# Kernel optimization log

Hardware: AMD Instinct MI355X
Metric: run time of the kernel (lower is better)

## Reference

```python
import jax, jax.numpy as jnp
import numpy as np
import math

B, Hs, Ws, C, NH, PP = 4, 32, 32, 1024, 16, 128
N = Hs * Ws
HD = C // NH
MAX_REL = 32
ROPE_THETA = 10000.0


def _gelu(t):
    return jax.nn.gelu(t, approximate=False)  # torch nn.GELU default (erf)


def _rope(x):
    # x: [B, nh, N, hd]; interleaved even/odd rotation as in _apply_rope
    hd = x.shape[-1]
    inv_freq = 1.0 / (ROPE_THETA ** (jnp.arange(0, hd, 2, dtype=jnp.float32) / hd))
    pos = jnp.arange(x.shape[-2], dtype=jnp.float32)
    ang = pos[:, None] * inv_freq[None, :]  # [N, hd/2]
    sin, cos = jnp.sin(ang), jnp.cos(ang)
    x1, x2 = x[..., 0::2], x[..., 1::2]
    return jnp.stack([x1 * cos - x2 * sin, x2 * cos + x1 * sin], axis=-1).reshape(x.shape)


def _rel_bias(table):
    # static index computation (numpy), gather from learned table -> [1, NH, N, N]
    coords = np.arange(Hs)
    cy, cx = np.meshgrid(coords, coords, indexing='ij')
    cf = np.stack([cy.reshape(-1), cx.reshape(-1)])  # [2, N]
    rel = cf[:, :, None] - cf[:, None, :]            # [2, N, N]
    idx = (rel[0] + MAX_REL - 1) * (2 * MAX_REL - 1) + (rel[1] + MAX_REL - 1)
    return table[jnp.asarray(idx.reshape(-1))].reshape(N, N, NH).transpose(2, 0, 1)[None]


def setup_inputs() -> dict:
    key = jax.random.key(0)
    ks = iter(jax.random.split(key, 40))
    def w(shape, s=0.02):
        return jax.random.normal(next(ks), shape, jnp.float32) * s
    return dict(
        x=jax.random.normal(next(ks), (B, N, C), jnp.float32),
        plucker=jax.random.normal(next(ks), (B, Hs, Ws, 6), jnp.float32),
        w_qkv=w((C, 3 * C)), w_self_proj=w((C, C)), b_self_proj=jnp.zeros((C,), jnp.float32),
        pl_w1=w((6, 2 * PP)), pl_b1=jnp.zeros((2 * PP,), jnp.float32),
        pl_w2=w((2 * PP, PP)), pl_b2=jnp.zeros((PP,), jnp.float32),
        pl_w3=w((PP, PP)), pl_b3=jnp.zeros((PP,), jnp.float32),
        w_cq=w((C, C)), w_pk=w((PP, C)), w_pv=w((PP, C)),
        w_cross_proj=w((C, C)), b_cross_proj=jnp.zeros((C,), jnp.float32),
        ray_dir_bias=w((NH,)),
        ds_w1=w((6, 4 * NH)), ds_b1=jnp.zeros((4 * NH,), jnp.float32),
        ds_w2=w((4 * NH, NH)), ds_b2=jnp.zeros((NH,), jnp.float32),
        gb_w1=w((2 * PP, C // 2)), gb_b1=jnp.zeros((C // 2,), jnp.float32),
        gb_w2=w((C // 2, NH)), gb_b2=jnp.zeros((NH,), jnp.float32),
        rel_table=w(((2 * MAX_REL - 1) ** 2, NH)),
        gfe_w1=w((C + PP, C)), gfe_b1=jnp.zeros((C,), jnp.float32),
        gfe_w2=w((C, C)), gfe_b2=jnp.zeros((C,), jnp.float32),
    )


def reference(x, plucker, w_qkv, w_self_proj, b_self_proj,
              pl_w1, pl_b1, pl_w2, pl_b2, pl_w3, pl_b3,
              w_cq, w_pk, w_pv, w_cross_proj, b_cross_proj,
              ray_dir_bias, ds_w1, ds_b1, ds_w2, ds_b2,
              gb_w1, gb_b1, gb_w2, gb_b2, rel_table,
              gfe_w1, gfe_b1, gfe_w2, gfe_b2):
    scale = HD ** (-0.5)
    pl_flat = plucker.reshape(B, N, 6)

    # ---- self attention with RoPE + relative position bias ----
    qkv = (x @ w_qkv).reshape(B, N, 3, NH, HD).transpose(2, 0, 3, 1, 4)
    q, k, v = qkv[0], qkv[1], qkv[2]          # [B, NH, N, HD]
    q, k = _rope(q), _rope(k)
    attn = jnp.einsum('bhnd,bhmd->bhnm', q, k) * scale + _rel_bias(rel_table)
    attn = jax.nn.softmax(attn, axis=-1)
    sa = jnp.einsum('bhnm,bhmd->bhnd', attn, v).transpose(0, 2, 1, 3).reshape(B, N, C)
    sa = sa @ w_self_proj + b_self_proj

    # ---- plucker mlp embedding ----
    pp = _gelu(pl_flat @ pl_w1 + pl_b1)
    pp = _gelu(pp @ pl_w2 + pl_b2)
    pp = pp @ pl_w3 + pl_b3                   # [B, N, PP]

    # ---- cross attention (features -> plucker) with geometric biases ----
    cq = (sa @ w_cq).reshape(B, N, NH, HD).transpose(0, 2, 1, 3)
    ck = (pp @ w_pk).reshape(B, N, NH, HD).transpose(0, 2, 1, 3)
    cv = (pp @ w_pv).reshape(B, N, NH, HD).transpose(0, 2, 1, 3)
    cq, ck = _rope(cq), _rope(ck)
    ca = jnp.einsum('bhnd,bhmd->bhnm', cq, ck) * scale

    # ray direction similarity bias (per-head learned weight)
    d = pl_flat[..., :3]
    dn = d / jnp.maximum(jnp.linalg.norm(d, axis=-1, keepdims=True), 1e-12)
    sim = jnp.einsum('bnd,bmd->bnm', dn, dn)  # [B, N, N]
    ca = ca + sim[:, None, :, :] * ray_dir_bias[None, :, None, None]

    # distance-aware per-query multiplicative scale
    ds = jnp.tanh(_gelu(pl_flat @ ds_w1 + ds_b1) @ ds_w2 + ds_b2)  # [B, N, NH]
    ca = ca * (1.0 + ds.transpose(0, 2, 1)[..., None])

    # geometric attention bias from spatial diffs of plucker features
    p2 = pp.reshape(B, Hs, Ws, PP)
    hdiff = jnp.pad(jnp.abs(p2[:, :, 1:] - p2[:, :, :-1]), ((0, 0), (0, 0), (0, 1), (0, 0)))
    vdiff = jnp.pad(jnp.abs(p2[:, 1:] - p2[:, :-1]), ((0, 0), (0, 1), (0, 0), (0, 0)))
    sd = jnp.concatenate([hdiff, vdiff], axis=-1).reshape(B, N, 2 * PP)
    gb = jnp.tanh(_gelu(sd @ gb_w1 + gb_b1) @ gb_w2 + gb_b2)  # [B, N, NH]
    ca = ca + gb.transpose(0, 2, 1)[:, :, None, :]            # broadcast over queries

    ca = jax.nn.softmax(ca, axis=-1)
    co = jnp.einsum('bhnm,bhmd->bhnd', ca, cv).transpose(0, 2, 1, 3).reshape(B, N, C)
    co = co @ w_cross_proj + b_cross_proj

    # ---- geometric feature enhancement + residual ----
    enh = _gelu(jnp.concatenate([co, pp], axis=-1) @ gfe_w1 + gfe_b1) @ gfe_w2 + gfe_b2
    return enh + x
```

## Files before the change

### kernel.cpp

```cpp
#include <hip/hip_runtime.h>
#include <math.h>

#define B_ 4
#define N_ 1024
#define C_ 1024
#define NH_ 16
#define HD_ 64
#define PP_ 128
#define LOG2E 1.4426950408889634f

typedef __bf16 bf16;
typedef __attribute__((ext_vector_type(8))) __bf16 bf16x8;
typedef __attribute__((ext_vector_type(4))) __bf16 bf16x4;
typedef __attribute__((ext_vector_type(4))) float f32x4;

#define MFMA_BF16(a, b, c) __builtin_amdgcn_mfma_f32_16x16x32_bf16((a), (b), (c), 0, 0, 0)

__device__ __forceinline__ float gelu_f(float x) {
    return 0.5f * x * (1.0f + erff(x * 0.70710678118654752f));
}

__device__ __forceinline__ void gload16(const void* g, void* l) {
    __builtin_amdgcn_global_load_lds(
        (const __attribute__((address_space(1))) void*)g,
        (__attribute__((address_space(3))) void*)l, 16, 0, 0);
}

__device__ __forceinline__ void stage64(const bf16* __restrict__ g, int pitchB,
                                        bf16* lds, int t) {
    int row = t >> 3, c = t & 7;
    const char* src = (const char*)g + (size_t)row * pitchB + ((c ^ (row & 7)) << 4);
    gload16(src, lds + (size_t)(t & 448) * 8);
}

__device__ __forceinline__ void stage32(const bf16* __restrict__ g, bf16* lds, int t) {
    if (t < 256) {
        int row = t >> 3, c = t & 7;
        const char* src = (const char*)g + (size_t)row * 128 + ((c ^ (row & 7)) << 4);
        gload16(src, lds + (size_t)(t & 192) * 8);
    }
}

__device__ __forceinline__ bf16x8 lds8_swz(const bf16* lds, int row, int colb) {
    return *reinterpret_cast<const bf16x8*>(
        (const char*)lds + row * 128 + (colb ^ ((row & 7) << 4)));
}

__device__ __forceinline__ bf16x8 lds8_ke(const bf16* lds, int kr, int g) {
    int r = kr >> 1;
    int ch = ((kr & 1) * 4 + g) ^ (r & 7);
    return *reinterpret_cast<const bf16x8*>((const char*)lds + r * 128 + (ch << 4));
}

__global__ __launch_bounds__(256) void rope_tab_k(float2* __restrict__ rt)
{
    int g = blockIdx.x * 256 + threadIdx.x;
    const int n = g >> 5, i = g & 31;
    const float inv = powf(10000.0f, -(float)(2 * i) / 64.0f);
    const float ang = (float)n * inv;
    rt[g] = make_float2(cosf(ang), sinf(ang));
}

__global__ __launch_bounds__(256) void relT_k(const float* __restrict__ rel_table,
                                              float* __restrict__ relT)
{
    int g = blockIdx.x * 256 + threadIdx.x;
    if (g >= 16 * 3969) return;
    int h = g / 3969, idx = g - h * 3969;
    relT[g] = rel_table[idx * 16 + h];
}

struct TJobs {
    const float* src[11];
    bf16* dst[11];
    int K[11];
    int N[11];
};

__global__ __launch_bounds__(256) void tcast_k(TJobs J)
{
    const int j = blockIdx.z;
    const int Kd = J.K[j], Nd = J.N[j];
    const int n0 = blockIdx.x * 32, k0 = blockIdx.y * 32;
    if (n0 >= Nd || k0 >= Kd) return;
    __shared__ float tl[32][33];
    const int t = threadIdx.x, tx = t & 31, ty = t >> 5;
    const float* src = J.src[j];
    bf16* dst = J.dst[j];
    #pragma unroll
    for (int r = 0; r < 4; ++r) {
        int kk = ty + r * 8;
        tl[kk][tx] = src[(size_t)(k0 + kk) * Nd + n0 + tx];
    }
    __syncthreads();
    #pragma unroll
    for (int r = 0; r < 4; ++r) {
        int nn = ty + r * 8;
        dst[(size_t)(n0 + nn) * Kd + k0 + tx] = (bf16)tl[tx][nn];
    }
}

__global__ __launch_bounds__(256) void cast_rm(const float* __restrict__ in,
                                               bf16* __restrict__ out, int n4)
{
    int g = blockIdx.x * 256 + threadIdx.x;
    if (g >= n4) return;
    float4 v = reinterpret_cast<const float4*>(in)[g];
    bf16x4 o = {(bf16)v.x, (bf16)v.y, (bf16)v.z, (bf16)v.w};
    reinterpret_cast<bf16x4*>(out)[g] = o;
}

template<int NI, int BK>
__global__ __launch_bounds__(256) void gemm_m(
    const bf16* __restrict__ A, const bf16* __restrict__ A2,
    const bf16* __restrict__ Bt, const bf16* __restrict__ Bt2,
    const float* __restrict__ bias, const float* __restrict__ resid,
    void* __restrict__ out0, void* __restrict__ out1, void* __restrict__ out2,
    const float2* __restrict__ rtab,
    int M, int N, int K, int K1A, int K1B, int epi, int act_gelu, float scale)
{
    __shared__ bf16 As[2][128 * BK];
    __shared__ bf16 Bs[2][NI * 32 * BK];
    const int t = threadIdx.x;
    const int w = t >> 6, lane = t & 63;
    const int row0 = blockIdx.y * 128, col0 = blockIdx.x * (NI * 32);
    const int wm = w >> 1, wn = w & 1;
    const int K2A = K - K1A, K2B = K - K1B;
    f32x4 acc[4][NI];
    #pragma unroll
    for (int mi = 0; mi < 4; ++mi)
        #pragma unroll
        for (int ni = 0; ni < NI; ++ni)
            acc[mi][ni] = (f32x4){0.f, 0.f, 0.f, 0.f};

    #define STAGE_AB32(k0, buf)                                                \
        {                                                                      \
            _Pragma("unroll")                                                  \
            for (int r = 0; r < 2; ++r) {                                      \
                int c = r * 256 + t;                                           \
                int rr = c >> 2, koff = (c & 3) * 8;                           \
                const bf16* srca = ((k0) < K1A)                                \
                    ? A + (size_t)(row0 + rr) * K1A + (k0) + koff              \
                    : A2 + (size_t)(row0 + rr) * K2A + ((k0) - K1A) + koff;    \
                gload16(srca, As[buf] + (size_t)(r * 256 + (t & 192)) * 8);    \
            }                                                                  \
            _Pragma("unroll")                                                  \
            for (int r = 0; r < NI / 2; ++r) {                                 \
                int c = r * 256 + t;                                           \
                int rr = c >> 2, koff = (c & 3) * 8;                           \
                const bf16* srcb = ((k0) < K1B)                                \
                    ? Bt + (size_t)(col0 + rr) * K1B + (k0) + koff             \
                    : Bt2 + (size_t)(col0 + rr) * K2B + ((k0) - K1B) + koff;   \
                gload16(srcb, Bs[buf] + (size_t)(r * 256 + (t & 192)) * 8);    \
            }                                                                  \
        }

    #define STAGE_AB64(k0, buf)                                                \
        {                                                                      \
            const bf16* abase; int apitch;                                     \
            if ((k0) < K1A) { abase = A + (k0); apitch = K1A; }                \
            else            { abase = A2 + ((k0) - K1A); apitch = K2A; }       \
            _Pragma("unroll")                                                  \
            for (int r = 0; r < 4; ++r) {                                      \
                int c = r * 256 + t;                                           \
                int rr = c >> 3, cc = c & 7;                                   \
                const char* srca = (const char*)(abase + (size_t)(row0 + rr) * apitch) \
                                   + ((cc ^ (rr & 7)) << 4);                   \
                gload16(srca, As[buf] + (size_t)(r * 256 + (t & 192)) * 8);    \
            }                                                                  \
            const bf16* bbase; int bpitch;                                     \
            if ((k0) < K1B) { bbase = Bt + (k0); bpitch = K1B; }               \
            else            { bbase = Bt2 + ((k0) - K1B); bpitch = K2B; }      \
            _Pragma("unroll")                                                  \
            for (int r = 0; r < NI; ++r) {                                     \
                int c = r * 256 + t;                                           \
                int rr = c >> 3, cc = c & 7;                                   \
                const char* srcb = (const char*)(bbase + (size_t)(col0 + rr) * bpitch) \
                                   + ((cc ^ (rr & 7)) << 4);                   \
                gload16(srcb, Bs[buf] + (size_t)(r * 256 + (t & 192)) * 8);    \
            }                                                                  \
        }

    int cur = 0;
    const int nk = K / BK;
    if constexpr (BK == 32) {
        STAGE_AB32(0, 0);
        __syncthreads();
        for (int kk = 0; kk < nk; ++kk) {
            if (kk + 1 < nk) STAGE_AB32((kk + 1) * 32, cur ^ 1);
            bf16x8 af[4], bfv[NI];
            #pragma unroll
            for (int mi = 0; mi < 4; ++mi)
                af[mi] = *reinterpret_cast<const bf16x8*>(
                    As[cur] + (wm * 64 + mi * 16 + (lane & 15)) * 32 + (lane >> 4) * 8);
            #pragma unroll
            for (int ni = 0; ni < NI; ++ni)
                bfv[ni] = *reinterpret_cast<const bf16x8*>(
                    Bs[cur] + (wn * (NI * 16) + ni * 16 + (lane & 15)) * 32 + (lane >> 4) * 8);
            #pragma unroll
            for (int mi = 0; mi < 4; ++mi)
                #pragma unroll
                for (int ni = 0; ni < NI; ++ni)
                    acc[mi][ni] = MFMA_BF16(af[mi], bfv[ni], acc[mi][ni]);
            __syncthreads();
            cur ^= 1;
        }
    } else {
        STAGE_AB64(0, 0);
        __syncthreads();
        for (int kk = 0; kk < nk; ++kk) {
            if (kk + 1 < nk) STAGE_AB64((kk + 1) * 64, cur ^ 1);
            bf16x8 af[4][2], bfv[NI][2];
            #pragma unroll
            for (int mi = 0; mi < 4; ++mi)
                #pragma unroll
                for (int kh = 0; kh < 2; ++kh)
                    af[mi][kh] = lds8_swz(As[cur], wm * 64 + mi * 16 + (lane & 15),
                                          kh * 64 + (lane >> 4) * 16);
            #pragma unroll
            for (int ni = 0; ni < NI; ++ni)
                #pragma unroll
                for (int kh = 0; kh < 2; ++kh)
                    bfv[ni][kh] = lds8_swz(Bs[cur], wn * (NI * 16) + ni * 16 + (lane & 15),
                                           kh * 64 + (lane >> 4) * 16);
            #pragma unroll
            for (int kh = 0; kh < 2; ++kh)
                #pragma unroll
                for (int mi = 0; mi < 4; ++mi)
                    #pragma unroll
                    for (int ni = 0; ni < NI; ++ni)
                        acc[mi][ni] = MFMA_BF16(af[mi][kh], bfv[ni][kh], acc[mi][ni]);
            __syncthreads();
            cur ^= 1;
        }
    }
    #undef STAGE_AB32
    #undef STAGE_AB64

    #pragma unroll
    for (int mi = 0; mi < 4; ++mi) {
        #pragma unroll
        for (int ni = 0; ni < NI; ++ni) {
            const int col = col0 + wn * (NI * 16) + ni * 16 + (lane & 15);
            if (epi <= 1 || epi == 5) {
                const float bv = bias ? bias[col] : 0.f;
                #pragma unroll
                for (int j = 0; j < 4; ++j) {
                    const int row = row0 + wm * 64 + mi * 16 + (lane >> 4) * 4 + j;
                    float v = acc[mi][ni][j] + bv;
                    if (act_gelu) v = gelu_f(v);
                    if (epi == 0) {
                        if (resid) v += resid[(size_t)row * N + col];
                        ((float*)out0)[(size_t)row * N + col] = v;
                    } else if (epi == 1) {
                        ((bf16*)out0)[(size_t)row * N + col] = (bf16)v;
                    } else {
                        ((float*)out0)[(size_t)row * N + col] = v;
                        ((bf16*)out1)[(size_t)row * N + col] = (bf16)v;
                    }
                }
            } else if (epi == 2) {
                const int reg = col >> 10;
                const int h = (col >> 6) & 15, d = col & 63;
                if (reg <= 1) {
                    bf16* dst = reg == 0 ? (bf16*)out0 : (bf16*)out1;
                    const float sc = reg == 0 ? scale : 1.0f;
                    #pragma unroll
                    for (int j = 0; j < 4; ++j) {
                        const int row = row0 + wm * 64 + mi * 16 + (lane >> 4) * 4 + j;
                        const int b = row >> 10, n = row & 1023;
                        float v = acc[mi][ni][j];
                        float pv = __shfl_xor(v, 1);
                        float2 cs = rtab[(n << 5) + (d >> 1)];
                        float o = (d & 1) == 0 ? v * cs.x - pv * cs.y
                                               : v * cs.x + pv * cs.y;
                        dst[((size_t)((b * 16 + h) * 1024 + n)) * 64 + d] = (bf16)(o * sc);
                    }
                } else {
                    bf16x4 o4;
                    #pragma unroll
                    for (int j = 0; j < 4; ++j) o4[j] = (bf16)acc[mi][ni][j];
                    const int row = row0 + wm * 64 + mi * 16 + (lane >> 4) * 4;
                    const int b = row >> 10, n = row & 1023;
                    *reinterpret_cast<bf16x4*>(
                        (bf16*)out2 + ((size_t)((b * 16 + h) * 64 + d)) * 1024 + n) = o4;
                }
            } else if (epi == 3 || epi == 6) {
                const int h = (col >> 6) & 15, d = col & 63;
                #pragma unroll
                for (int j = 0; j < 4; ++j) {
                    const int row = row0 + wm * 64 + mi * 16 + (lane >> 4) * 4 + j;
                    const int b = row >> 10, n = row & 1023;
                    float v = acc[mi][ni][j];
                    float pv = __shfl_xor(v, 1);
                    float2 cs = rtab[(n << 5) + (d >> 1)];
                    float o = (d & 1) == 0 ? v * cs.x - pv * cs.y
                                           : v * cs.x + pv * cs.y;
                    float sc = scale;
                    if (epi == 6) sc *= 1.0f + resid[(size_t)row * 16 + h];
                    ((bf16*)out0)[((size_t)((b * 16 + h) * 1024 + n)) * 64 + d] = (bf16)(o * sc);
                }
            } else {
                const int h = (col >> 6) & 15, d = col & 63;
                bf16x4 o4;
                #pragma unroll
                for (int j = 0; j < 4; ++j) o4[j] = (bf16)acc[mi][ni][j];
                const int row = row0 + wm * 64 + mi * 16 + (lane >> 4) * 4;
                const int b = row >> 10, n = row & 1023;
                *reinterpret_cast<bf16x4*>(
                    (bf16*)out0 + ((size_t)((b * 16 + h) * 64 + d)) * 1024 + n) = o4;
            }
        }
    }
}

__global__ __launch_bounds__(256) void extfill_k(
    const float* __restrict__ dn, const float* __restrict__ ds,
    const float* __restrict__ gb, const float* __restrict__ rdb,
    bf16* __restrict__ qe, bf16* __restrict__ ke)
{
    int g = blockIdx.x * 256 + threadIdx.x;
    if (g >= 65536) return;
    const int bh = g >> 10, n = g & 1023;
    const int b = bh >> 4, h = bh & 15;
    const size_t rn = (size_t)b * 1024 + n;
    const float c1 = rdb[h] * LOG2E * (1.0f + ds[rn * 16 + h]);
    const float dx = dn[rn * 4], dy = dn[rn * 4 + 1], dz = dn[rn * 4 + 2];
    bf16x8 z = {};
    bf16x8 q0 = z, k0 = z;
    q0[0] = (bf16)(dx * c1); q0[1] = (bf16)(dy * c1); q0[2] = (bf16)(dz * c1); q0[3] = (bf16)1.0f;
    k0[0] = (bf16)dx; k0[1] = (bf16)dy; k0[2] = (bf16)dz; k0[3] = (bf16)(gb[rn * 16 + h] * LOG2E);
    bf16x8* qp = reinterpret_cast<bf16x8*>(qe + (size_t)g * 32);
    bf16x8* kp = reinterpret_cast<bf16x8*>(ke + (size_t)g * 32);
    qp[0] = q0; qp[1] = z; qp[2] = z; qp[3] = z;
    kp[0] = k0; kp[1] = z; kp[2] = z; kp[3] = z;
}

__device__ __forceinline__ void attn_bid(int bid, int& bh, int& r0t) {
    const int xcd = bid & 7, s = bid >> 3;
    bh = (s >> 3) * 8 + xcd;
    r0t = s & 7;
}

__global__ __launch_bounds__(512) void attn_self_m(
    const bf16* __restrict__ qb, const bf16* __restrict__ kb, const bf16* __restrict__ vtb,
    const float* __restrict__ relT, bf16* __restrict__ sab)
{
    __shared__ bf16 Ks[2][64 * 64];
    __shared__ bf16 Vs[2][80 * 64];
    __shared__ bf16 Ps[128 * 64];
    __shared__ float relb[2][320];
    const int t = threadIdx.x, w = t >> 6, lane = t & 63;
    int bh, r0t;
    attn_bid(blockIdx.x, bh, r0t);
    const int b = bh >> 4, h = bh & 15, r0 = r0t * 128;
    const float* relTh = relT + h * 3969;
    const int y0 = r0 >> 5;

    {
        const bf16* g = qb + ((size_t)bh * 1024 + r0) * 64;
        #pragma unroll
        for (int r = 0; r < 2; ++r) {
            int i = r * 512 + t;
            int row = i >> 3, c = i & 7;
            const char* src = (const char*)g + (size_t)row * 128 + ((c ^ (row & 7)) << 4);
            gload16(src, Ps + (size_t)(r * 512 + (t & 448)) * 8);
        }
    }
    __syncthreads();
    bf16x8 aq[2];
    {
        const int qr = w * 16 + (lane & 15);
        aq[0] = lds8_swz(Ps, qr, (lane >> 4) * 16);
        aq[1] = lds8_swz(Ps, qr, 64 + (lane >> 4) * 16);
    }
    for (int i = t; i < 2048; i += 512) {
        int buf = i >> 10, idx = i & 1023;
        int row = 64 + (idx >> 6), col = idx & 63;
        Vs[buf][row * 64 + col] = (row == 64) ? (bf16)1.0f : (bf16)0.0f;
    }
    __syncthreads();
    stage64(kb + (size_t)bh * 65536, 128, Ks[0], t);
    stage64(vtb + (size_t)bh * 65536, 2048, Vs[0], t);
    if (t < 320) relb[0][t] = LOG2E * relTh[(y0 + 30 + (t >> 6)) * 63 + min(t & 63, 62)];

    float m_run[4];
    f32x4 of[4], ofe;
    #pragma unroll
    for (int j = 0; j < 4; ++j) m_run[j] = -3e38f;
    #pragma unroll
    for (int dt = 0; dt < 4; ++dt) of[dt] = (f32x4){0.f, 0.f, 0.f, 0.f};
    ofe = (f32x4){0.f, 0.f, 0.f, 0.f};

    const int qrow_lo = (lane >> 4) * 4;
    int dybase[4];
    #pragma unroll
    for (int j = 0; j < 4; ++j) {
        int qg = r0 + w * 16 + qrow_lo + j;
        dybase[j] = (((qg >> 5) - y0) + 1) * 64 + (qg & 31) + 31;
    }
    __syncthreads();

    int cur = 0;
    for (int mt = 0; mt < 16; ++mt) {
        if (mt < 15) {
            stage64(kb + (size_t)bh * 65536 + (size_t)(mt + 1) * 64 * 64, 128, Ks[cur ^ 1], t);
            stage64(vtb + (size_t)bh * 65536 + (size_t)(mt + 1) * 64, 2048, Vs[cur ^ 1], t);
            if (t < 320)
                relb[cur ^ 1][t] = LOG2E * relTh[(y0 - 2 * (mt + 1) + 30 + (t >> 6)) * 63 + min(t & 63, 62)];
        }
        f32x4 sf[4];
        __builtin_amdgcn_s_setprio(1);
        #pragma unroll
        for (int ct = 0; ct < 4; ++ct) {
            const int kr = ct * 16 + (lane & 15);
            f32x4 a = (f32x4){0.f, 0.f, 0.f, 0.f};
            a = MFMA_BF16(aq[0], lds8_swz(Ks[cur], kr, (lane >> 4) * 16), a);
            a = MFMA_BF16(aq[1], lds8_swz(Ks[cur], kr, 64 + (lane >> 4) * 16), a);
            sf[ct] = a;
        }
        __builtin_amdgcn_s_setprio(0);
        float p[4][4], lmax[4];
        #pragma unroll
        for (int j = 0; j < 4; ++j) lmax[j] = -3e38f;
        #pragma unroll
        for (int ct = 0; ct < 4; ++ct) {
            const int xm = (ct & 1) * 16 + (lane & 15);
            const int ro = (ct >> 1) * 64 + xm;
            #pragma unroll
            for (int j = 0; j < 4; ++j) {
                float s = sf[ct][j] + relb[cur][dybase[j] - ro];
                p[ct][j] = s;
                lmax[j] = fmaxf(lmax[j], s);
            }
        }
        bool need = false;
        #pragma unroll
        for (int j = 0; j < 4; ++j) need |= (lmax[j] > m_run[j] + 8.0f);
        if (__any(need)) {
            float mx[4], alpha[4];
            #pragma unroll
            for (int j = 0; j < 4; ++j) mx[j] = lmax[j];
            #pragma unroll
            for (int d = 1; d < 16; d <<= 1)
                #pragma unroll
                for (int j = 0; j < 4; ++j) mx[j] = fmaxf(mx[j], __shfl_xor(mx[j], d));
            #pragma unroll
            for (int j = 0; j < 4; ++j) {
                float mn = fmaxf(m_run[j], mx[j]);
                alpha[j] = exp2f(m_run[j] - mn);
                m_run[j] = mn;
            }
            #pragma unroll
            for (int dt = 0; dt < 4; ++dt)
                #pragma unroll
                for (int j = 0; j < 4; ++j) of[dt][j] *= alpha[j];
            #pragma unroll
            for (int j = 0; j < 4; ++j) ofe[j] *= alpha[j];
        }
        #pragma unroll
        for (int ct = 0; ct < 4; ++ct)
            #pragma unroll
            for (int j = 0; j < 4; ++j)
                p[ct][j] = exp2f(p[ct][j] - m_run[j]);
        #pragma unroll
        for (int ct = 0; ct < 4; ++ct)
            #pragma unroll
            for (int j = 0; j < 4; ++j) {
                const int prow = w * 16 + qrow_lo + j;
                const int ch = (ct * 2 + ((lane & 15) >> 3)) ^ (prow & 7);
                *reinterpret_cast<bf16*>((char*)Ps + prow * 128 + (ch << 4) + (lane & 7) * 2)
                    = (bf16)p[ct][j];
            }
        asm volatile("s_waitcnt lgkmcnt(0)" ::: "memory");
        __builtin_amdgcn_sched_barrier(0);
        bf16x8 ap0 = lds8_swz(Ps, w * 16 + (lane & 15), (lane >> 4) * 16);
        bf16x8 ap1 = lds8_swz(Ps, w * 16 + (lane & 15), 64 + (lane >> 4) * 16);
        __builtin_amdgcn_s_setprio(1);
        #pragma unroll
        for (int dt = 0; dt < 4; ++dt) {
            const int vr = dt * 16 + (lane & 15);
            of[dt] = MFMA_BF16(ap0, lds8_swz(Vs[cur], vr, (lane >> 4) * 16), of[dt]);
            of[dt] = MFMA_BF16(ap1, lds8_swz(Vs[cur], vr, 64 + (lane >> 4) * 16), of[dt]);
        }
        {
            const int vr = 64 + (lane & 15);
            ofe = MFMA_BF16(ap0, lds8_swz(Vs[cur], vr, (lane >> 4) * 16), ofe);
            ofe = MFMA_BF16(ap1, lds8_swz(Vs[cur], vr, 64 + (lane >> 4) * 16), ofe);
        }
        __builtin_amdgcn_s_setprio(0);
        __syncthreads();
        cur ^= 1;
    }
    float inv[4];
    #pragma unroll
    for (int j = 0; j < 4; ++j) inv[j] = 1.f / __shfl(ofe[j], lane & 48);
    #pragma unroll
    for (int dt = 0; dt < 4; ++dt)
        #pragma unroll
        for (int j = 0; j < 4; ++j)
            sab[((size_t)(b * N_ + r0 + w * 16 + qrow_lo + j)) * C_ + h * 64 + dt * 16 + (lane & 15)] =
                (bf16)(of[dt][j] * inv[j]);
}

__global__ __launch_bounds__(512) void attn_cross_m(
    const bf16* __restrict__ cq, const bf16* __restrict__ qe,
    const bf16* __restrict__ ck, const bf16* __restrict__ ke,
    const bf16* __restrict__ cvt, bf16* __restrict__ cob)
{
    __shared__ bf16 Ks[2][64 * 64];
    __shared__ bf16 Ke[2][32 * 64];
    __shared__ bf16 Vs[2][80 * 64];
    __shared__ bf16 Ps[128 * 64];
    const int t = threadIdx.x, w = t >> 6, lane = t & 63;
    int bh, r0t;
    attn_bid(blockIdx.x, bh, r0t);
    const int b = bh >> 4, h = bh & 15, r0 = r0t * 128;

    {
        const bf16* g = cq + ((size_t)bh * 1024 + r0) * 64;
        #pragma unroll
        for (int r = 0; r < 2; ++r) {
            int i = r * 512 + t;
            int row = i >> 3, c = i & 7;
            const char* src = (const char*)g + (size_t)row * 128 + ((c ^ (row & 7)) << 4);
            gload16(src, Ps + (size_t)(r * 512 + (t & 448)) * 8);
        }
    }
    stage64(qe + ((size_t)bh * 1024 + r0) * 32, 128, Ks[0], t);
    __syncthreads();
    bf16x8 aq[2], aqe;
    {
        const int qr = w * 16 + (lane & 15);
        aq[0] = lds8_swz(Ps, qr, (lane >> 4) * 16);
        aq[1] = lds8_swz(Ps, qr, 64 + (lane >> 4) * 16);
        aqe = lds8_ke(Ks[0], qr, lane >> 4);
    }
    for (int i = t; i < 2048; i += 512) {
        int buf = i >> 10, idx = i & 1023;
        int row = 64 + (idx >> 6), col = idx & 63;
        Vs[buf][row * 64 + col] = (row == 64) ? (bf16)1.0f : (bf16)0.0f;
    }
    __syncthreads();
    stage64(ck + (size_t)bh * 65536, 128, Ks[0], t);
    stage32(ke + (size_t)bh * 32768, Ke[0], t);
    stage64(cvt + (size_t)bh * 65536, 2048, Vs[0], t);

    float m_run[4];
    f32x4 of[4], ofe;
    #pragma unroll
    for (int j = 0; j < 4; ++j) m_run[j] = -3e38f;
    #pragma unroll
    for (int dt = 0; dt < 4; ++dt) of[dt] = (f32x4){0.f, 0.f, 0.f, 0.f};
    ofe = (f32x4){0.f, 0.f, 0.f, 0.f};
    const int qrow_lo = (lane >> 4) * 4;
    __syncthreads();

    int cur = 0;
    for (int mt = 0; mt < 16; ++mt) {
        if (mt < 15) {
            stage64(ck + (size_t)bh * 65536 + (size_t)(mt + 1) * 64 * 64, 128, Ks[cur ^ 1], t);
            stage32(ke + (size_t)bh * 32768 + (size_t)(mt + 1) * 64 * 32, Ke[cur ^ 1], t);
            stage64(cvt + (size_t)bh * 65536 + (size_t)(mt + 1) * 64, 2048, Vs[cur ^ 1], t);
        }
        f32x4 sf[4];
        __builtin_amdgcn_s_setprio(1);
        #pragma unroll
        for (int ct = 0; ct < 4; ++ct) {
            const int kr = ct * 16 + (lane & 15);
            f32x4 a = (f32x4){0.f, 0.f, 0.f, 0.f};
            a = MFMA_BF16(aq[0], lds8_swz(Ks[cur], kr, (lane >> 4) * 16), a);
            a = MFMA_BF16(aq[1], lds8_swz(Ks[cur], kr, 64 + (lane >> 4) * 16), a);
            a = MFMA_BF16(aqe, lds8_ke(Ke[cur], kr, lane >> 4), a);
            sf[ct] = a;
        }
        __builtin_amdgcn_s_setprio(0);
        float lmax[4];
        #pragma unroll
        for (int j = 0; j < 4; ++j)
            lmax[j] = fmaxf(fmaxf(sf[0][j], sf[1][j]), fmaxf(sf[2][j], sf[3][j]));
        bool need = false;
        #pragma unroll
        for (int j = 0; j < 4; ++j) need |= (lmax[j] > m_run[j] + 8.0f);
        if (__any(need)) {
            float mx[4], alpha[4];
            #pragma unroll
            for (int j = 0; j < 4; ++j) mx[j] = lmax[j];
            #pragma unroll
            for (int d = 1; d < 16; d <<= 1)
                #pragma unroll
                for (int j = 0; j < 4; ++j) mx[j] = fmaxf(mx[j], __shfl_xor(mx[j], d));
            #pragma unroll
            for (int j = 0; j < 4; ++j) {
                float mn = fmaxf(m_run[j], mx[j]);
                alpha[j] = exp2f(m_run[j] - mn);
                m_run[j] = mn;
            }
            #pragma unroll
            for (int dt = 0; dt < 4; ++dt)
                #pragma unroll
                for (int j = 0; j < 4; ++j) of[dt][j] *= alpha[j];
            #pragma unroll
            for (int j = 0; j < 4; ++j) ofe[j] *= alpha[j];
        }
        #pragma unroll
        for (int ct = 0; ct < 4; ++ct)
            #pragma unroll
            for (int j = 0; j < 4; ++j)
                sf[ct][j] = exp2f(sf[ct][j] - m_run[j]);
        #pragma unroll
        for (int ct = 0; ct < 4; ++ct)
            #pragma unroll
            for (int j = 0; j < 4; ++j) {
                const int prow = w * 16 + qrow_lo + j;
                const int ch = (ct * 2 + ((lane & 15) >> 3)) ^ (prow & 7);
                *reinterpret_cast<bf16*>((char*)Ps + prow * 128 + (ch << 4) + (lane & 7) * 2)
                    = (bf16)sf[ct][j];
            }
        asm volatile("s_waitcnt lgkmcnt(0)" ::: "memory");
        __builtin_amdgcn_sched_barrier(0);
        bf16x8 ap0 = lds8_swz(Ps, w * 16 + (lane & 15), (lane >> 4) * 16);
        bf16x8 ap1 = lds8_swz(Ps, w * 16 + (lane & 15), 64 + (lane >> 4) * 16);
        __builtin_amdgcn_s_setprio(1);
        #pragma unroll
        for (int dt = 0; dt < 4; ++dt) {
            const int vr = dt * 16 + (lane & 15);
            of[dt] = MFMA_BF16(ap0, lds8_swz(Vs[cur], vr, (lane >> 4) * 16), of[dt]);
            of[dt] = MFMA_BF16(ap1, lds8_swz(Vs[cur], vr, 64 + (lane >> 4) * 16), of[dt]);
        }
        {
            const int vr = 64 + (lane & 15);
            ofe = MFMA_BF16(ap0, lds8_swz(Vs[cur], vr, (lane >> 4) * 16), ofe);
            ofe = MFMA_BF16(ap1, lds8_swz(Vs[cur], vr, 64 + (lane >> 4) * 16), ofe);
        }
        __builtin_amdgcn_s_setprio(0);
        __syncthreads();
        cur ^= 1;
    }
    float inv[4];
    #pragma unroll
    for (int j = 0; j < 4; ++j) inv[j] = 1.f / __shfl(ofe[j], lane & 48);
    #pragma unroll
    for (int dt = 0; dt < 4; ++dt)
        #pragma unroll
        for (int j = 0; j < 4; ++j)
            cob[((size_t)(b * N_ + r0 + w * 16 + qrow_lo + j)) * C_ + h * 64 + dt * 16 + (lane & 15)] =
                (bf16)(of[dt][j] * inv[j]);
}

__global__ __launch_bounds__(256) void plucker1_k(
    const float* __restrict__ pl,
    const float* __restrict__ w1, const float* __restrict__ b1,
    const float* __restrict__ dw1, const float* __restrict__ db1,
    const float* __restrict__ dw2, const float* __restrict__ db2,
    bf16* __restrict__ h1b, float* __restrict__ ds, float* __restrict__ dn)
{
    const int t = threadIdx.x;
    __shared__ float plr[6];
    __shared__ float dh[64];
    #pragma unroll 1
    for (int rr = 0; rr < 4; ++rr) {
        const int row = blockIdx.x * 4 + rr;
        if (t < 6) plr[t] = pl[(size_t)row * 6 + t];
        __syncthreads();
        {
            float a = b1[t];
            #pragma unroll
            for (int j = 0; j < 6; ++j) a = fmaf(plr[j], w1[j * 256 + t], a);
            h1b[(size_t)row * 256 + t] = (bf16)gelu_f(a);
        }
        if (t < 64) {
            float d = db1[t];
            #pragma unroll
            for (int j = 0; j < 6; ++j) d = fmaf(plr[j], dw1[j * 64 + t], d);
            dh[t] = gelu_f(d);
        }
        if (t == 0) {
            float x = plr[0], y = plr[1], z = plr[2];
            float nrm = fmaxf(sqrtf(x * x + y * y + z * z), 1e-12f);
            dn[(size_t)row * 4 + 0] = x / nrm;
            dn[(size_t)row * 4 + 1] = y / nrm;
            dn[(size_t)row * 4 + 2] = z / nrm;
            dn[(size_t)row * 4 + 3] = 0.f;
        }
        __syncthreads();
        if (t < 16) {
            float d = db2[t];
            #pragma unroll 8
            for (int j = 0; j < 64; ++j) d = fmaf(dh[j], dw2[j * 16 + t], d);
            ds[(size_t)row * 16 + t] = tanhf(d);
        }
        __syncthreads();
    }
}

__global__ __launch_bounds__(256) void sd_k(const float* __restrict__ pp, bf16* __restrict__ sd)
{
    int g = blockIdx.x * 256 + threadIdx.x;
    if (g >= B_ * N_ * PP_) return;
    const int c = g & 127;
    const int rown = g >> 7;
    const int n = rown & (N_ - 1);
    const int xx = n & 31, yy = (n >> 5) & 31;
    const float cur = pp[g];
    const float hd = (xx < 31) ? fabsf(pp[g + PP_] - cur) : 0.f;
    const float vd = (yy < 31) ? fabsf(pp[g + 32 * PP_] - cur) : 0.f;
    sd[(size_t)rown * 256 + c] = (bf16)hd;
    sd[(size_t)rown * 256 + 128 + c] = (bf16)vd;
}

__global__ __launch_bounds__(256) void gb2_k(
    const bf16* __restrict__ h, const float* __restrict__ w2,
    const float* __restrict__ b2, float* __restrict__ gbv)
{
    __shared__ float w2s[512 * 16];
    const int t = threadIdx.x;
    for (int i = t; i < 8192; i += 256) w2s[i] = w2[i];
    __syncthreads();
    const int row = blockIdx.x * 16 + (t >> 4);
    const int col = t & 15;
    const bf16* hr = h + (size_t)row * 512;
    float acc = b2[col];
    #pragma unroll 8
    for (int j = 0; j < 512; ++j)
        acc = fmaf((float)hr[j], w2s[j * 16 + col], acc);
    gbv[(size_t)row * 16 + col] = tanhf(acc);
}

extern "C" void kernel_launch(void* const* d_in, const int* in_sizes, int n_in,
                              void* d_out, int out_size, void* d_ws, size_t ws_size,
                              hipStream_t stream)
{
    const float* x     = (const float*)d_in[0];
    const float* pl    = (const float*)d_in[1];
    const float* w_qkv = (const float*)d_in[2];
    const float* w_sp  = (const float*)d_in[3];
    const float* b_sp  = (const float*)d_in[4];
    const float* pl_w1 = (const float*)d_in[5];
    const float* pl_b1 = (const float*)d_in[6];
    const float* pl_w2 = (const float*)d_in[7];
    const float* pl_b2 = (const float*)d_in[8];
    const float* pl_w3 = (const float*)d_in[9];
    const float* pl_b3 = (const float*)d_in[10];
    const float* w_cq  = (const float*)d_in[11];
    const float* w_pk  = (const float*)d_in[12];
    const float* w_pv  = (const float*)d_in[13];
    const float* w_cp  = (const float*)d_in[14];
    const float* b_cp  = (const float*)d_in[15];
    const float* rdb   = (const float*)d_in[16];
    const float* ds_w1 = (const float*)d_in[17];
    const float* ds_b1 = (const float*)d_in[18];
    const float* ds_w2 = (const float*)d_in[19];
    const float* ds_b2 = (const float*)d_in[20];
    const float* gb_w1 = (const float*)d_in[21];
    const float* gb_b1 = (const float*)d_in[22];
    const float* gb_w2 = (const float*)d_in[23];
    const float* gb_b2 = (const float*)d_in[24];
    const float* rel_t = (const float*)d_in[25];
    const float* gfw1  = (const float*)d_in[26];
    const float* gfb1  = (const float*)d_in[27];
    const float* gfw2  = (const float*)d_in[28];
    const float* gfb2  = (const float*)d_in[29];

    char* W = (char*)d_ws;
    float* out = (float*)d_out;
    const size_t MB = 1ull << 20;
    const size_t KB = 1024;

    bf16* qb     = (bf16*)(W + 0);
    bf16* kb     = (bf16*)(W + 8 * MB);
    bf16* vtb    = (bf16*)(W + 16 * MB);
    bf16* cqb    = qb;
    bf16* ckb    = kb;
    bf16* cvtb   = vtb;
    bf16* xb     = (bf16*)(W + 24 * MB);
    bf16* wqkvT  = (bf16*)(W + 32 * MB);
    bf16* wspT   = (bf16*)(W + 38 * MB);
    bf16* wcqT   = (bf16*)(W + 40 * MB);
    bf16* wpkT   = (bf16*)(W + 42 * MB);
    bf16* wpvT   = (bf16*)(W + 42 * MB + 256 * KB);
    bf16* wcpT   = (bf16*)(W + 43 * MB);
    bf16* gfw1T  = (bf16*)(W + 45 * MB);
    bf16* gfw2T  = (bf16*)(W + 48 * MB);
    bf16* plw2T  = (bf16*)(W + 50 * MB);
    bf16* plw3T  = (bf16*)(W + 50 * MB + 64 * KB);
    bf16* gbw1T  = (bf16*)(W + 50 * MB + 128 * KB);
    bf16* sab    = (bf16*)(W + 51 * MB);
    bf16* cob    = sab;
    bf16* sapb   = (bf16*)(W + 59 * MB);
    bf16* copb   = sapb;
    float* pp    = (float*)(W + 67 * MB);
    bf16* ppb    = (bf16*)(W + 69 * MB);
    bf16* sdb16  = (bf16*)(W + 70 * MB);
    bf16* h1b    = (bf16*)(W + 72 * MB);
    bf16* h2b    = (bf16*)(W + 74 * MB);
    bf16* gbh    = (bf16*)(W + 75 * MB);
    float* dsb   = (float*)(W + 79 * MB);
    float* dnb   = (float*)(W + 79 * MB + 256 * KB);
    float* gbb   = (float*)(W + 79 * MB + 320 * KB);
    float2* rtab = (float2*)(W + 80 * MB);
    float* relTb = (float*)(W + 80 * MB + 256 * KB);
    bf16* hidb   = (bf16*)(W + 81 * MB);
    bf16* qeb    = (bf16*)(W + 89 * MB);
    bf16* keb    = (bf16*)(W + 93 * MB);

    const dim3 blk(256);

    TJobs J;
    J.src[0] = w_qkv; J.dst[0] = wqkvT; J.K[0] = 1024; J.N[0] = 3072;
    J.src[1] = w_sp;  J.dst[1] = wspT;  J.K[1] = 1024; J.N[1] = 1024;
    J.src[2] = w_cq;  J.dst[2] = wcqT;  J.K[2] = 1024; J.N[2] = 1024;
    J.src[3] = w_pk;  J.dst[3] = wpkT;  J.K[3] = 128;  J.N[3] = 1024;
    J.src[4] = w_pv;  J.dst[4] = wpvT;  J.K[4] = 128;  J.N[4] = 1024;
    J.src[5] = w_cp;  J.dst[5] = wcpT;  J.K[5] = 1024; J.N[5] = 1024;
    J.src[6] = gfw1;  J.dst[6] = gfw1T; J.K[6] = 1152; J.N[6] = 1024;
    J.src[7] = gfw2;  J.dst[7] = gfw2T; J.K[7] = 1024; J.N[7] = 1024;
    J.src[8] = pl_w2; J.dst[8] = plw2T; J.K[8] = 256;  J.N[8] = 128;
    J.src[9] = pl_w3; J.dst[9] = plw3T; J.K[9] = 128;  J.N[9] = 128;
    J.src[10]= gb_w1; J.dst[10]= gbw1T; J.K[10]= 256;  J.N[10]= 512;
    tcast_k<<<dim3(96, 36, 11), blk, 0, stream>>>(J);
    cast_rm<<<4096, blk, 0, stream>>>(x, xb, 1048576);
    rope_tab_k<<<128, blk, 0, stream>>>(rtab);
    relT_k<<<249, blk, 0, stream>>>(rel_t, relTb);

    gemm_m<2, 64><<<dim3(48, 32), blk, 0, stream>>>(xb, nullptr, wqkvT, nullptr, nullptr, nullptr,
        qb, kb, vtb, rtab, 4096, 3072, 1024, 1024, 1024, 2, 0, 0.125f * LOG2E);
    attn_self_m<<<512, dim3(512), 0, stream>>>(qb, kb, vtb, relTb, sab);
    gemm_m<2, 64><<<dim3(16, 32), blk, 0, stream>>>(sab, nullptr, wspT, nullptr, b_sp, nullptr,
        sapb, nullptr, nullptr, nullptr, 4096, 1024, 1024, 1024, 1024, 1, 0, 1.f);
    plucker1_k<<<1024, blk, 0, stream>>>(pl, pl_w1, pl_b1,
                                         ds_w1, ds_b1, ds_w2, ds_b2, h1b, dsb, dnb);
    gemm_m<2, 64><<<dim3(2, 32), blk, 0, stream>>>(h1b, nullptr, plw2T, nullptr, pl_b2, nullptr,
        h2b, nullptr, nullptr, nullptr, 4096, 128, 256, 256, 256, 1, 1, 1.f);
    gemm_m<2, 64><<<dim3(2, 32), blk, 0, stream>>>(h2b, nullptr, plw3T, nullptr, pl_b3, nullptr,
        pp, ppb, nullptr, nullptr, 4096, 128, 128, 128, 128, 5, 0, 1.f);
    sd_k<<<2048, blk, 0, stream>>>(pp, sdb16);
    gemm_m<2, 64><<<dim3(8, 32), blk, 0, stream>>>(sdb16, nullptr, gbw1T, nullptr, gb_b1, nullptr,
        gbh, nullptr, nullptr, nullptr, 4096, 512, 256, 256, 256, 1, 1, 1.f);
    gb2_k<<<256, blk, 0, stream>>>(gbh, gb_w2, gb_b2, gbb);
    gemm_m<2, 64><<<dim3(16, 32), blk, 0, stream>>>(sapb, nullptr, wcqT, nullptr, nullptr, dsb,
        cqb, nullptr, nullptr, rtab, 4096, 1024, 1024, 1024, 1024, 6, 0, 0.125f * LOG2E);
    gemm_m<2, 64><<<dim3(16, 32), blk, 0, stream>>>(ppb, nullptr, wpkT, nullptr, nullptr, nullptr,
        ckb, nullptr, nullptr, rtab, 4096, 1024, 128, 128, 128, 3, 0, 1.0f);
    gemm_m<2, 64><<<dim3(16, 32), blk, 0, stream>>>(ppb, nullptr, wpvT, nullptr, nullptr, nullptr,
        cvtb, nullptr, nullptr, nullptr, 4096, 1024, 128, 128, 128, 4, 0, 1.f);
    extfill_k<<<256, blk, 0, stream>>>(dnb, dsb, gbb, rdb, qeb, keb);
    attn_cross_m<<<512, dim3(512), 0, stream>>>(cqb, qeb, ckb, keb, cvtb, cob);
    gemm_m<2, 64><<<dim3(16, 32), blk, 0, stream>>>(cob, nullptr, wcpT, nullptr, b_cp, nullptr,
        copb, nullptr, nullptr, nullptr, 4096, 1024, 1024, 1024, 1024, 1, 0, 1.f);
    gemm_m<2, 64><<<dim3(16, 32), blk, 0, stream>>>(copb, ppb, gfw1T, nullptr, gfb1, nullptr,
        hidb, nullptr, nullptr, nullptr, 4096, 1024, 1152, 1024, 1152, 1, 1, 1.f);
    gemm_m<2, 64><<<dim3(16, 32), blk, 0, stream>>>(hidb, nullptr, gfw2T, nullptr, gfb2, x,
        out, nullptr, nullptr, nullptr, 4096, 1024, 1024, 1024, 1024, 0, 0, 1.f);
}
```

Measured before the change: 344.7 us.

## Fold self-proj into cross-query weights, merge pk/pv GEMMs, fuse extfill into gb2

Precomputes W_sp·W_cq and b_sp·W_cq so the self-attention output projection GEMM disappears and the cross-query GEMM reads the attention output directly. The pk and pv GEMMs are merged into one launch with a new epilogue that routes column halves to the rope-K and transposed-V outputs. The extfill kernel is folded into the gb2 kernel, and the attention kernels move the ones/zeros V extension into a separate LDS buffer and store relative bias in bf16. This removes a 4096x1024x1024 GEMM and several launches. In exchange it adds a small weight-product GEMM each call and changes rounding, since the folded weights are rounded to bf16 and the relative bias loses precision.

```diff
diff --git a/kernel.cpp b/kernel.cpp
--- a/kernel.cpp
+++ b/kernel.cpp
@@ -108,6 +108,23 @@
     float4 v = reinterpret_cast<const float4*>(in)[g];
     bf16x4 o = {(bf16)v.x, (bf16)v.y, (bf16)v.z, (bf16)v.w};
     reinterpret_cast<bf16x4*>(out)[g] = o;
+}
+
+__global__ __launch_bounds__(256) void bsc_k(const float* __restrict__ b_sp,
+                                             const float* __restrict__ w_cq,
+                                             float* __restrict__ bsc)
+{
+    __shared__ float red[4][64];
+    const int t = threadIdx.x;
+    const int c = blockIdx.x * 64 + (t & 63);
+    const int js = t >> 6;
+    float a = 0.f;
+    #pragma unroll 8
+    for (int j = js * 256; j < js * 256 + 256; ++j)
+        a = fmaf(b_sp[j], w_cq[(size_t)j * 1024 + c], a);
+    red[js][t & 63] = a;
+    __syncthreads();
+    if (t < 64) bsc[blockIdx.x * 64 + t] = red[0][t] + red[1][t] + red[2][t] + red[3][t];
 }
 
 template<int NI, int BK>
@@ -287,11 +304,12 @@
                 }
             } else if (epi == 3 || epi == 6) {
                 const int h = (col >> 6) & 15, d = col & 63;
+                const float bv = bias ? bias[col] : 0.f;
                 #pragma unroll
                 for (int j = 0; j < 4; ++j) {
                     const int row = row0 + wm * 64 + mi * 16 + (lane >> 4) * 4 + j;
                     const int b = row >> 10, n = row & 1023;
-                    float v = acc[mi][ni][j];
+                    float v = acc[mi][ni][j] + bv;
                     float pv = __shfl_xor(v, 1);
                     float2 cs = rtab[(n << 5) + (d >> 1)];
                     float o = (d & 1) == 0 ? v * cs.x - pv * cs.y
@@ -300,6 +318,30 @@
                     if (epi == 6) sc *= 1.0f + resid[(size_t)row * 16 + h];
                     ((bf16*)out0)[((size_t)((b * 16 + h) * 1024 + n)) * 64 + d] = (bf16)(o * sc);
                 }
+            } else if (epi == 7) {
+                const int reg = col >> 10;
+                const int h = (col >> 6) & 15, d = col & 63;
+                if (reg == 0) {
+                    #pragma unroll
+                    for (int j = 0; j < 4; ++j) {
+                        const int row = row0 + wm * 64 + mi * 16 + (lane >> 4) * 4 + j;
+                        const int b = row >> 10, n = row & 1023;
+                        float v = acc[mi][ni][j];
+                        float pv = __shfl_xor(v, 1);
+                        float2 cs = rtab[(n << 5) + (d >> 1)];
+                        float o = (d & 1) == 0 ? v * cs.x - pv * cs.y
+                                               : v * cs.x + pv * cs.y;
+                        ((bf16*)out0)[((size_t)((b * 16 + h) * 1024 + n)) * 64 + d] = (bf16)o;
+                    }
+                } else {
+                    bf16x4 o4;
+                    #pragma unroll
+                    for (int j = 0; j < 4; ++j) o4[j] = (bf16)acc[mi][ni][j];
+                    const int row = row0 + wm * 64 + mi * 16 + (lane >> 4) * 4;
+                    const int b = row >> 10, n = row & 1023;
+                    *reinterpret_cast<bf16x4*>(
+                        (bf16*)out2 + ((size_t)((b * 16 + h) * 64 + d)) * 1024 + n) = o4;
+                }
             } else {
                 const int h = (col >> 6) & 15, d = col & 63;
                 bf16x4 o4;
@@ -314,28 +356,6 @@
     }
 }
 
-__global__ __launch_bounds__(256) void extfill_k(
-    const float* __restrict__ dn, const float* __restrict__ ds,
-    const float* __restrict__ gb, const float* __restrict__ rdb,
-    bf16* __restrict__ qe, bf16* __restrict__ ke)
-{
-    int g = blockIdx.x * 256 + threadIdx.x;
-    if (g >= 65536) return;
-    const int bh = g >> 10, n = g & 1023;
-    const int b = bh >> 4, h = bh & 15;
-    const size_t rn = (size_t)b * 1024 + n;
-    const float c1 = rdb[h] * LOG2E * (1.0f + ds[rn * 16 + h]);
-    const float dx = dn[rn * 4], dy = dn[rn * 4 + 1], dz = dn[rn * 4 + 2];
-    bf16x8 z = {};
-    bf16x8 q0 = z, k0 = z;
-    q0[0] = (bf16)(dx * c1); q0[1] = (bf16)(dy * c1); q0[2] = (bf16)(dz * c1); q0[3] = (bf16)1.0f;
-    k0[0] = (bf16)dx; k0[1] = (bf16)dy; k0[2] = (bf16)dz; k0[3] = (bf16)(gb[rn * 16 + h] * LOG2E);
-    bf16x8* qp = reinterpret_cast<bf16x8*>(qe + (size_t)g * 32);
-    bf16x8* kp = reinterpret_cast<bf16x8*>(ke + (size_t)g * 32);
-    qp[0] = q0; qp[1] = z; qp[2] = z; qp[3] = z;
-    kp[0] = k0; kp[1] = z; kp[2] = z; kp[3] = z;
-}
-
 __device__ __forceinline__ void attn_bid(int bid, int& bh, int& r0t) {
     const int xcd = bid & 7, s = bid >> 3;
     bh = (s >> 3) * 8 + xcd;
@@ -347,9 +367,10 @@
     const float* __restrict__ relT, bf16* __restrict__ sab)
 {
     __shared__ bf16 Ks[2][64 * 64];
-    __shared__ bf16 Vs[2][80 * 64];
+    __shared__ bf16 Vs[2][64 * 64];
+    __shared__ bf16 Vext[16 * 64];
     __shared__ bf16 Ps[128 * 64];
-    __shared__ float relb[2][320];
+    __shared__ bf16 relb[2][320];
     const int t = threadIdx.x, w = t >> 6, lane = t & 63;
     int bh, r0t;
     attn_bid(blockIdx.x, bh, r0t);
@@ -374,15 +395,12 @@
         aq[0] = lds8_swz(Ps, qr, (lane >> 4) * 16);
         aq[1] = lds8_swz(Ps, qr, 64 + (lane >> 4) * 16);
     }
-    for (int i = t; i < 2048; i += 512) {
-        int buf = i >> 10, idx = i & 1023;
-        int row = 64 + (idx >> 6), col = idx & 63;
-        Vs[buf][row * 64 + col] = (row == 64) ? (bf16)1.0f : (bf16)0.0f;
-    }
+    for (int i = t; i < 1024; i += 512)
+        Vext[i] = ((i >> 6) == 0) ? (bf16)1.0f : (bf16)0.0f;
     __syncthreads();
     stage64(kb + (size_t)bh * 65536, 128, Ks[0], t);
     stage64(vtb + (size_t)bh * 65536, 2048, Vs[0], t);
-    if (t < 320) relb[0][t] = LOG2E * relTh[(y0 + 30 + (t >> 6)) * 63 + min(t & 63, 62)];
+    if (t < 320) relb[0][t] = (bf16)(LOG2E * relTh[(y0 + 30 + (t >> 6)) * 63 + min(t & 63, 62)]);
 
     float m_run[4];
     f32x4 of[4], ofe;
@@ -407,7 +425,7 @@
             stage64(kb + (size_t)bh * 65536 + (size_t)(mt + 1) * 64 * 64, 128, Ks[cur ^ 1], t);
             stage64(vtb + (size_t)bh * 65536 + (size_t)(mt + 1) * 64, 2048, Vs[cur ^ 1], t);
             if (t < 320)
-                relb[cur ^ 1][t] = LOG2E * relTh[(y0 - 2 * (mt + 1) + 30 + (t >> 6)) * 63 + min(t & 63, 62)];
+                relb[cur ^ 1][t] = (bf16)(LOG2E * relTh[(y0 - 2 * (mt + 1) + 30 + (t >> 6)) * 63 + min(t & 63, 62)]);
         }
         f32x4 sf[4];
         __builtin_amdgcn_s_setprio(1);
@@ -429,7 +447,7 @@
             const int ro = (ct >> 1) * 64 + xm;
             #pragma unroll
             for (int j = 0; j < 4; ++j) {
-                float s = sf[ct][j] + relb[cur][dybase[j] - ro];
+                float s = sf[ct][j] + (float)relb[cur][dybase[j] - ro];
                 p[ct][j] = s;
                 lmax[j] = fmaxf(lmax[j], s);
             }
@@ -484,9 +502,9 @@
             of[dt] = MFMA_BF16(ap1, lds8_swz(Vs[cur], vr, 64 + (lane >> 4) * 16), of[dt]);
         }
         {
-            const int vr = 64 + (lane & 15);
-            ofe = MFMA_BF16(ap0, lds8_swz(Vs[cur], vr, (lane >> 4) * 16), ofe);
-            ofe = MFMA_BF16(ap1, lds8_swz(Vs[cur], vr, 64 + (lane >> 4) * 16), ofe);
+            const int vr = lane & 15;
+            ofe = MFMA_BF16(ap0, lds8_swz(Vext, vr, (lane >> 4) * 16), ofe);
+            ofe = MFMA_BF16(ap1, lds8_swz(Vext, vr, 64 + (lane >> 4) * 16), ofe);
         }
         __builtin_amdgcn_s_setprio(0);
         __syncthreads();
@@ -510,7 +528,8 @@
 {
     __shared__ bf16 Ks[2][64 * 64];
     __shared__ bf16 Ke[2][32 * 64];
-    __shared__ bf16 Vs[2][80 * 64];
+    __shared__ bf16 Vs[2][64 * 64];
+    __shared__ bf16 Vext[16 * 64];
     __shared__ bf16 Ps[128 * 64];
     const int t = threadIdx.x, w = t >> 6, lane = t & 63;
     int bh, r0t;
@@ -536,11 +555,8 @@
         aq[1] = lds8_swz(Ps, qr, 64 + (lane >> 4) * 16);
         aqe = lds8_ke(Ks[0], qr, lane >> 4);
     }
-    for (int i = t; i < 2048; i += 512) {
-        int buf = i >> 10, idx = i & 1023;
-        int row = 64 + (idx >> 6), col = idx & 63;
-        Vs[buf][row * 64 + col] = (row == 64) ? (bf16)1.0f : (bf16)0.0f;
-    }
+    for (int i = t; i < 1024; i += 512)
+        Vext[i] = ((i >> 6) == 0) ? (bf16)1.0f : (bf16)0.0f;
     __syncthreads();
     stage64(ck + (size_t)bh * 65536, 128, Ks[0], t);
     stage32(ke + (size_t)bh * 32768, Ke[0], t);
@@ -629,9 +645,9 @@
             of[dt] = MFMA_BF16(ap1, lds8_swz(Vs[cur], vr, 64 + (lane >> 4) * 16), of[dt]);
         }
         {
-            const int vr = 64 + (lane & 15);
-            ofe = MFMA_BF16(ap0, lds8_swz(Vs[cur], vr, (lane >> 4) * 16), ofe);
-            ofe = MFMA_BF16(ap1, lds8_swz(Vs[cur], vr, 64 + (lane >> 4) * 16), ofe);
+            const int vr = lane & 15;
+            ofe = MFMA_BF16(ap0, lds8_swz(Vext, vr, (lane >> 4) * 16), ofe);
+            ofe = MFMA_BF16(ap1, lds8_swz(Vext, vr, 64 + (lane >> 4) * 16), ofe);
         }
         __builtin_amdgcn_s_setprio(0);
         __syncthreads();
@@ -709,22 +725,35 @@
     sd[(size_t)rown * 256 + 128 + c] = (bf16)vd;
 }
 
-__global__ __launch_bounds__(256) void gb2_k(
-    const bf16* __restrict__ h, const float* __restrict__ w2,
-    const float* __restrict__ b2, float* __restrict__ gbv)
+__global__ __launch_bounds__(256) void gb2x_k(
+    const bf16* __restrict__ h, const float* __restrict__ w2, const float* __restrict__ b2,
+    const float* __restrict__ dn, const float* __restrict__ ds, const float* __restrict__ rdb,
+    bf16* __restrict__ qe, bf16* __restrict__ ke)
 {
     __shared__ float w2s[512 * 16];
     const int t = threadIdx.x;
     for (int i = t; i < 8192; i += 256) w2s[i] = w2[i];
     __syncthreads();
     const int row = blockIdx.x * 16 + (t >> 4);
-    const int col = t & 15;
+    const int hh = t & 15;
     const bf16* hr = h + (size_t)row * 512;
-    float acc = b2[col];
+    float acc = b2[hh];
     #pragma unroll 8
     for (int j = 0; j < 512; ++j)
-        acc = fmaf((float)hr[j], w2s[j * 16 + col], acc);
-    gbv[(size_t)row * 16 + col] = tanhf(acc);
+        acc = fmaf((float)hr[j], w2s[j * 16 + hh], acc);
+    const float gbv = tanhf(acc);
+    const int b = row >> 10, n = row & 1023;
+    const float c1 = rdb[hh] * LOG2E * (1.0f + ds[(size_t)row * 16 + hh]);
+    const float dx = dn[(size_t)row * 4], dy = dn[(size_t)row * 4 + 1], dz = dn[(size_t)row * 4 + 2];
+    bf16x8 z = {};
+    bf16x8 q0 = z, k0 = z;
+    q0[0] = (bf16)(dx * c1); q0[1] = (bf16)(dy * c1); q0[2] = (bf16)(dz * c1); q0[3] = (bf16)1.0f;
+    k0[0] = (bf16)dx; k0[1] = (bf16)dy; k0[2] = (bf16)dz; k0[3] = (bf16)(gbv * LOG2E);
+    const size_t g = (size_t)(b * 16 + hh) * 1024 + n;
+    bf16x8* qp = reinterpret_cast<bf16x8*>(qe + g * 32);
+    bf16x8* kp = reinterpret_cast<bf16x8*>(ke + g * 32);
+    qp[0] = q0; qp[1] = z; qp[2] = z; qp[3] = z;
+    kp[0] = k0; kp[1] = z; kp[2] = z; kp[3] = z;
 }
 
 extern "C" void kernel_launch(void* const* d_in, const int* in_sizes, int n_in,
@@ -775,7 +804,6 @@
     bf16* cvtb   = vtb;
     bf16* xb     = (bf16*)(W + 24 * MB);
     bf16* wqkvT  = (bf16*)(W + 32 * MB);
-    bf16* wspT   = (bf16*)(W + 38 * MB);
     bf16* wcqT   = (bf16*)(W + 40 * MB);
     bf16* wpkT   = (bf16*)(W + 42 * MB);
     bf16* wpvT   = (bf16*)(W + 42 * MB + 256 * KB);
@@ -787,8 +815,7 @@
     bf16* gbw1T  = (bf16*)(W + 50 * MB + 128 * KB);
     bf16* sab    = (bf16*)(W + 51 * MB);
     bf16* cob    = sab;
-    bf16* sapb   = (bf16*)(W + 59 * MB);
-    bf16* copb   = sapb;
+    bf16* copb   = (bf16*)(W + 59 * MB);
     float* pp    = (float*)(W + 67 * MB);
     bf16* ppb    = (bf16*)(W + 69 * MB);
     bf16* sdb16  = (bf16*)(W + 70 * MB);
@@ -797,37 +824,41 @@
     bf16* gbh    = (bf16*)(W + 75 * MB);
     float* dsb   = (float*)(W + 79 * MB);
     float* dnb   = (float*)(W + 79 * MB + 256 * KB);
-    float* gbb   = (float*)(W + 79 * MB + 320 * KB);
     float2* rtab = (float2*)(W + 80 * MB);
     float* relTb = (float*)(W + 80 * MB + 256 * KB);
     bf16* hidb   = (bf16*)(W + 81 * MB);
     bf16* qeb    = (bf16*)(W + 89 * MB);
     bf16* keb    = (bf16*)(W + 93 * MB);
+    bf16* wspB   = (bf16*)(W + 97 * MB);
+    bf16* wscT   = (bf16*)(W + 99 * MB);
+    float* bscb  = (float*)(W + 101 * MB);
 
     const dim3 blk(256);
 
     TJobs J;
     J.src[0] = w_qkv; J.dst[0] = wqkvT; J.K[0] = 1024; J.N[0] = 3072;
-    J.src[1] = w_sp;  J.dst[1] = wspT;  J.K[1] = 1024; J.N[1] = 1024;
-    J.src[2] = w_cq;  J.dst[2] = wcqT;  J.K[2] = 1024; J.N[2] = 1024;
-    J.src[3] = w_pk;  J.dst[3] = wpkT;  J.K[3] = 128;  J.N[3] = 1024;
-    J.src[4] = w_pv;  J.dst[4] = wpvT;  J.K[4] = 128;  J.N[4] = 1024;
-    J.src[5] = w_cp;  J.dst[5] = wcpT;  J.K[5] = 1024; J.N[5] = 1024;
-    J.src[6] = gfw1;  J.dst[6] = gfw1T; J.K[6] = 1152; J.N[6] = 1024;
-    J.src[7] = gfw2;  J.dst[7] = gfw2T; J.K[7] = 1024; J.N[7] = 1024;
-    J.src[8] = pl_w2; J.dst[8] = plw2T; J.K[8] = 256;  J.N[8] = 128;
-    J.src[9] = pl_w3; J.dst[9] = plw3T; J.K[9] = 128;  J.N[9] = 128;
-    J.src[10]= gb_w1; J.dst[10]= gbw1T; J.K[10]= 256;  J.N[10]= 512;
+    J.src[1] = w_cq;  J.dst[1] = wcqT;  J.K[1] = 1024; J.N[1] = 1024;
+    J.src[2] = w_pk;  J.dst[2] = wpkT;  J.K[2] = 128;  J.N[2] = 1024;
+    J.src[3] = w_pv;  J.dst[3] = wpvT;  J.K[3] = 128;  J.N[3] = 1024;
+    J.src[4] = w_cp;  J.dst[4] = wcpT;  J.K[4] = 1024; J.N[4] = 1024;
+    J.src[5] = gfw1;  J.dst[5] = gfw1T; J.K[5] = 1152; J.N[5] = 1024;
+    J.src[6] = gfw2;  J.dst[6] = gfw2T; J.K[6] = 1024; J.N[6] = 1024;
+    J.src[7] = pl_w2; J.dst[7] = plw2T; J.K[7] = 256;  J.N[7] = 128;
+    J.src[8] = pl_w3; J.dst[8] = plw3T; J.K[8] = 128;  J.N[8] = 128;
+    J.src[9] = gb_w1; J.dst[9] = gbw1T; J.K[9] = 256;  J.N[9] = 512;
+    J.src[10]= w_qkv; J.dst[10]= wqkvT; J.K[10]= 0;    J.N[10]= 0;
     tcast_k<<<dim3(96, 36, 11), blk, 0, stream>>>(J);
     cast_rm<<<4096, blk, 0, stream>>>(x, xb, 1048576);
+    cast_rm<<<1024, blk, 0, stream>>>(w_sp, wspB, 262144);
     rope_tab_k<<<128, blk, 0, stream>>>(rtab);
     relT_k<<<249, blk, 0, stream>>>(rel_t, relTb);
+    bsc_k<<<16, blk, 0, stream>>>(b_sp, w_cq, bscb);
+    gemm_m<2, 64><<<dim3(16, 8), blk, 0, stream>>>(wcqT, nullptr, wspB, nullptr, nullptr, nullptr,
+        wscT, nullptr, nullptr, nullptr, 1024, 1024, 1024, 1024, 1024, 1, 0, 1.f);
 
     gemm_m<2, 64><<<dim3(48, 32), blk, 0, stream>>>(xb, nullptr, wqkvT, nullptr, nullptr, nullptr,
         qb, kb, vtb, rtab, 4096, 3072, 1024, 1024, 1024, 2, 0, 0.125f * LOG2E);
     attn_self_m<<<512, dim3(512), 0, stream>>>(qb, kb, vtb, relTb, sab);
-    gemm_m<2, 64><<<dim3(16, 32), blk, 0, stream>>>(sab, nullptr, wspT, nullptr, b_sp, nullptr,
-        sapb, nullptr, nullptr, nullptr, 4096, 1024, 1024, 1024, 1024, 1, 0, 1.f);
     plucker1_k<<<1024, blk, 0, stream>>>(pl, pl_w1, pl_b1,
                                          ds_w1, ds_b1, ds_w2, ds_b2, h1b, dsb, dnb);
     gemm_m<2, 64><<<dim3(2, 32), blk, 0, stream>>>(h1b, nullptr, plw2T, nullptr, pl_b2, nullptr,
@@ -837,14 +868,11 @@
     sd_k<<<2048, blk, 0, stream>>>(pp, sdb16);
     gemm_m<2, 64><<<dim3(8, 32), blk, 0, stream>>>(sdb16, nullptr, gbw1T, nullptr, gb_b1, nullptr,
         gbh, nullptr, nullptr, nullptr, 4096, 512, 256, 256, 256, 1, 1, 1.f);
-    gb2_k<<<256, blk, 0, stream>>>(gbh, gb_w2, gb_b2, gbb);
-    gemm_m<2, 64><<<dim3(16, 32), blk, 0, stream>>>(sapb, nullptr, wcqT, nullptr, nullptr, dsb,
+    gb2x_k<<<256, blk, 0, stream>>>(gbh, gb_w2, gb_b2, dnb, dsb, rdb, qeb, keb);
+    gemm_m<2, 64><<<dim3(16, 32), blk, 0, stream>>>(sab, nullptr, wscT, nullptr, bscb, dsb,
         cqb, nullptr, nullptr, rtab, 4096, 1024, 1024, 1024, 1024, 6, 0, 0.125f * LOG2E);
-    gemm_m<2, 64><<<dim3(16, 32), blk, 0, stream>>>(ppb, nullptr, wpkT, nullptr, nullptr, nullptr,
-        ckb, nullptr, nullptr, rtab, 4096, 1024, 128, 128, 128, 3, 0, 1.0f);
-    gemm_m<2, 64><<<dim3(16, 32), blk, 0, stream>>>(ppb, nullptr, wpvT, nullptr, nullptr, nullptr,
-        cvtb, nullptr, nullptr, nullptr, 4096, 1024, 128, 128, 128, 4, 0, 1.f);
-    extfill_k<<<256, blk, 0, stream>>>(dnb, dsb, gbb, rdb, qeb, keb);
+    gemm_m<2, 64><<<dim3(32, 32), blk, 0, stream>>>(ppb, nullptr, wpkT, nullptr, nullptr, nullptr,
+        ckb, nullptr, cvtb, rtab, 4096, 2048, 128, 128, 128, 7, 0, 1.f);
     attn_cross_m<<<512, dim3(512), 0, stream>>>(cqb, qeb, ckb, keb, cvtb, cob);
     gemm_m<2, 64><<<dim3(16, 32), blk, 0, stream>>>(cob, nullptr, wcpT, nullptr, b_cp, nullptr,
         copb, nullptr, nullptr, nullptr, 4096, 1024, 1024, 1024, 1024, 1, 0, 1.f);
```

Result: slower. 367.9 us (+6.7%).
